# Kernel optimization log

Hardware: AMD Instinct MI355X
Metric: run time of the kernel (lower is better)

Reference implementation:

```python
import jax, jax.numpy as jnp
import numpy as np

D_MODEL = 2048
N_HEADS = 16
HEAD_DIM = D_MODEL // N_HEADS


def setup_inputs() -> dict:
    key = jax.random.key(0)
    k_x, k_wqkv, k_bqkv, k_wo, k_bo = jax.random.split(key, 5)
    B, T = 4, 1024
    s_in = 1.0 / np.sqrt(D_MODEL)
    return {
        "x": jax.random.normal(k_x, (B, T, D_MODEL), dtype=jnp.float32),
        "w_qkv": jax.random.uniform(k_wqkv, (D_MODEL, 3 * D_MODEL), jnp.float32, -s_in, s_in),
        "b_qkv": jax.random.uniform(k_bqkv, (3 * D_MODEL,), jnp.float32, -s_in, s_in),
        "w_out": jax.random.uniform(k_wo, (D_MODEL, D_MODEL), jnp.float32, -s_in, s_in),
        "b_out": jax.random.uniform(k_bo, (D_MODEL,), jnp.float32, -s_in, s_in),
    }


def reference(x, w_qkv, b_qkv, w_out, b_out) -> jnp.ndarray:
    B, T, C = x.shape
    qkv = x @ w_qkv + b_qkv                      # [B, T, 3C]
    q, k, v = jnp.split(qkv, 3, axis=-1)
    # [B, H, T, Dh]
    q = q.reshape(B, T, N_HEADS, HEAD_DIM).transpose(0, 2, 1, 3)
    k = k.reshape(B, T, N_HEADS, HEAD_DIM).transpose(0, 2, 1, 3)
    v = v.reshape(B, T, N_HEADS, HEAD_DIM).transpose(0, 2, 1, 3)
    scale = 1.0 / np.sqrt(HEAD_DIM).astype(np.float32)
    att = jnp.einsum("bhqd,bhkd->bhqk", q, k) * scale   # [B, H, T, T]
    causal = jnp.tril(jnp.ones((T, T), dtype=bool))
    att = jnp.where(causal, att, -jnp.inf)
    att = jax.nn.softmax(att, axis=-1)
    out = jnp.einsum("bhqk,bhkd->bhqd", att, v)          # [B, H, T, Dh]
    out = out.transpose(0, 2, 1, 3).reshape(B, T, C)
    return out @ w_out + b_out
```

## Files before the change

### kernel.cpp

```cpp
#include <hip/hip_runtime.h>
#include <hip/hip_bf16.h>
#include <math.h>

#define DM    2048
#define DQKV  6144
#define NH    16
#define DH    128
#define TT    1024
#define BB    4

typedef __bf16 bf16_t;
typedef __bf16 bf16x4 __attribute__((ext_vector_type(4)));
typedef __bf16 bf16x8 __attribute__((ext_vector_type(8)));
typedef float  f32x4  __attribute__((ext_vector_type(4)));

__device__ __forceinline__ void async16(const void* g, void* lds) {
  __builtin_amdgcn_global_load_lds(
      (const __attribute__((address_space(1))) unsigned int*)g,
      (__attribute__((address_space(3))) unsigned int*)lds, 16, 0, 0);
}

__global__ __launch_bounds__(256) void cast_kernel(const float* __restrict__ X,
                                                   bf16_t* __restrict__ Xb) {
  const size_t i = ((size_t)blockIdx.x * 256 + threadIdx.x) * 8;
  float4 a = *(const float4*)(X + i);
  float4 b = *(const float4*)(X + i + 4);
  bf16x8 o = {(bf16_t)a.x, (bf16_t)a.y, (bf16_t)a.z, (bf16_t)a.w,
              (bf16_t)b.x, (bf16_t)b.y, (bf16_t)b.z, (bf16_t)b.w};
  *(bf16x8*)(Xb + i) = o;
}

__global__ __launch_bounds__(256) void transpose_cast_kernel(
    const float* __restrict__ W, bf16_t* __restrict__ Wt, int K, int N) {
  __shared__ bf16_t tile[64][72];
  const int tid = threadIdx.x;
  const int tk = blockIdx.y * 64, tn = blockIdx.x * 64;
  {
    int r = tid >> 2, c0 = (tid & 3) * 16;
    const float* src = W + (size_t)(tk + r) * N + tn + c0;
#pragma unroll
    for (int j = 0; j < 4; ++j) {
      float4 v = *(const float4*)(src + j * 4);
      tile[r][c0 + j * 4 + 0] = (bf16_t)v.x;
      tile[r][c0 + j * 4 + 1] = (bf16_t)v.y;
      tile[r][c0 + j * 4 + 2] = (bf16_t)v.z;
      tile[r][c0 + j * 4 + 3] = (bf16_t)v.w;
    }
  }
  __syncthreads();
  {
    int n = tid >> 2, c0 = (tid & 3) * 16;
    bf16_t* dst = Wt + (size_t)(tn + n) * K + tk + c0;
#pragma unroll
    for (int j = 0; j < 4; ++j) {
      bf16x4 t = {tile[c0 + j * 4 + 0][n], tile[c0 + j * 4 + 1][n],
                  tile[c0 + j * 4 + 2][n], tile[c0 + j * 4 + 3][n]};
      *(bf16x4*)(dst + j * 4) = t;
    }
  }
}

__global__ __launch_bounds__(256) void v_transpose_kernel(
    const bf16_t* __restrict__ qkv, bf16_t* __restrict__ Vt_g) {
  __shared__ bf16_t tile[64][72];
  const int tid = threadIdx.x;
  const int dt = blockIdx.x;
  const int tt = blockIdx.y;
  const int bh = blockIdx.z;
  const int b = bh >> 4, h = bh & 15;
  {
    int r = tid >> 2, c0 = (tid & 3) * 16;
    const bf16_t* src =
        qkv + (size_t)(b * TT + tt * 64 + r) * DQKV + 2 * DM + h * DH + dt * 64 + c0;
    *(bf16x8*)&tile[r][c0]     = *(const bf16x8*)(src);
    *(bf16x8*)&tile[r][c0 + 8] = *(const bf16x8*)(src + 8);
  }
  __syncthreads();
  {
    int n = tid >> 2, c0 = (tid & 3) * 16;
    bf16_t* dst = Vt_g + (size_t)(bh * DH + dt * 64 + n) * TT + tt * 64 + c0;
#pragma unroll
    for (int j = 0; j < 4; ++j) {
      bf16x4 t = {tile[c0 + j * 4 + 0][n], tile[c0 + j * 4 + 1][n],
                  tile[c0 + j * 4 + 2][n], tile[c0 + j * 4 + 3][n]};
      *(bf16x4*)(dst + j * 4) = t;
    }
  }
}

template <bool OUT_BF16>
__global__ __launch_bounds__(256) void gemm_bt_kernel(
    const bf16_t* __restrict__ A, const bf16_t* __restrict__ Bt,
    const float* __restrict__ bias, void* __restrict__ out,
    int M, int N, int K) {
  __shared__ __align__(16) bf16_t As[128 * 64];
  __shared__ __align__(16) bf16_t Bs[128 * 64];

  const int tid  = threadIdx.x;
  const int lane = tid & 63;
  const int wave = tid >> 6;
  const int ln   = lane & 15;
  const int quad = lane >> 4;
  const int bm = blockIdx.y, bn = blockIdx.x;
  const int m0 = (wave >> 1) * 64;
  const int n0 = (wave & 1) * 64;

  const bf16_t* Abase = A + (size_t)bm * 128 * K;
  const bf16_t* Bbase = Bt + (size_t)bn * 128 * K;

  f32x4 acc[4][4] = {};

  const int kIters = K >> 6;
  for (int kt = 0; kt < kIters; ++kt) {
    __syncthreads();
#pragma unroll
    for (int j = 0; j < 4; ++j) {
      const int fb  = j * 256 + wave * 64;
      const int f   = fb + lane;
      const int row = f >> 3, c = f & 7;
      const int gc  = c ^ (row & 7);
      const size_t goff = (size_t)row * K + kt * 64 + gc * 8;
      async16(Abase + goff, (char*)As + fb * 16);
      async16(Bbase + goff, (char*)Bs + fb * 16);
    }
    __syncthreads();

#pragma unroll
    for (int ks = 0; ks < 2; ++ks) {
      bf16x8 af[4], bfr[4];
#pragma unroll
      for (int i = 0; i < 4; ++i) {
        int row = m0 + 16 * i + ln;
        int c = (ks * 4 + quad) ^ (row & 7);
        af[i] = *(const bf16x8*)((const char*)As + ((row * 8 + c) << 4));
      }
#pragma unroll
      for (int jj = 0; jj < 4; ++jj) {
        int row = n0 + 16 * jj + ln;
        int c = (ks * 4 + quad) ^ (row & 7);
        bfr[jj] = *(const bf16x8*)((const char*)Bs + ((row * 8 + c) << 4));
      }
#pragma unroll
      for (int i = 0; i < 4; ++i)
#pragma unroll
        for (int jj = 0; jj < 4; ++jj)
          acc[i][jj] = __builtin_amdgcn_mfma_f32_16x16x32_bf16(
              af[i], bfr[jj], acc[i][jj], 0, 0, 0);
    }
  }

#pragma unroll
  for (int i = 0; i < 4; ++i) {
    int rowg = bm * 128 + m0 + 16 * i + quad * 4;
#pragma unroll
    for (int j = 0; j < 4; ++j) {
      int colg = bn * 128 + n0 + 16 * j + ln;
      float bb = bias[colg];
#pragma unroll
      for (int r = 0; r < 4; ++r) {
        float val = acc[i][j][r] + bb;
        if (OUT_BF16)
          ((bf16_t*)out)[(size_t)(rowg + r) * N + colg] = (bf16_t)val;
        else
          ((float*)out)[(size_t)(rowg + r) * N + colg] = val;
      }
    }
  }
}

__global__ __launch_bounds__(256) void attn_kernel(
    const bf16_t* __restrict__ qkv, const bf16_t* __restrict__ Vt_g,
    bf16_t* __restrict__ attout) {
  const int bx = blockIdx.x;
  const int p  = bx & 7;
  const int h  = (bx >> 3) & 15;
  const int b  = bx >> 7;
  const int bh = b * NH + h;
  const int tid  = threadIdx.x;
  const int lane = tid & 63;
  const int wave = tid >> 6;
  const int ln   = lane & 15;
  const int quad = lane >> 4;

  __shared__ __align__(16) bf16_t Ks[2][64 * 128];
  __shared__ __align__(16) bf16_t Vs[2][128 * 64];
  __shared__ __align__(16) bf16_t Ps[4 * 16 * 64];

  const float scale = 0.08838834764831845f;

  auto prefetch = [&](int c, int bufi) {
    const int kc = c * 64;
#pragma unroll
    for (int j = 0; j < 4; ++j) {
      const int fb = j * 256 + wave * 64;
      const int l  = fb + lane;
      {
        const int row = l >> 4, cc = l & 15;
        const int gc  = cc ^ (row & 7);
        const bf16_t* g =
            qkv + (size_t)(b * TT + kc + row) * DQKV + DM + h * DH + gc * 8;
        async16(g, (char*)Ks[bufi] + fb * 16);
      }
      {
        const int d = l >> 3, cc = l & 7;
        const int gc = cc ^ (d & 7);
        const bf16_t* g = Vt_g + (size_t)(bh * DH + d) * TT + kc + gc * 8;
        async16(g, (char*)Vs[bufi] + fb * 16);
      }
    }
  };

  int buf = 0;
  prefetch(0, 0);

  for (int half = 0; half < 2; ++half) {
    const int qt = half ? (15 - p) : p;
    const int q0 = qt * 64 + wave * 16;

    bf16x8 aq[4];
    {
      const bf16_t* qrow = qkv + (size_t)(b * TT + q0 + ln) * DQKV + h * DH;
#pragma unroll
      for (int kt = 0; kt < 4; ++kt)
        aq[kt] = *(const bf16x8*)(qrow + kt * 32 + quad * 8);
    }

    f32x4 o[8] = {};
    float mrow[4], lrow[4];
#pragma unroll
    for (int r = 0; r < 4; ++r) { mrow[r] = -1e30f; lrow[r] = 0.f; }

    for (int c = 0; c <= qt; ++c) {
      const int kc = c * 64;
      __syncthreads();

      if (c < qt)                prefetch(c + 1, buf ^ 1);
      else if (half == 0)        prefetch(0,     buf ^ 1);

      const bf16_t* KsB = Ks[buf];
      const bf16_t* VsB = Vs[buf];

      f32x4 sacc[4];
#pragma unroll
      for (int jt = 0; jt < 4; ++jt) {
        sacc[jt] = (f32x4){0.f, 0.f, 0.f, 0.f};
#pragma unroll
        for (int kt = 0; kt < 4; ++kt) {
          const int row = jt * 16 + ln;
          const int sc  = (kt * 4 + quad) ^ (row & 7);
          bf16x8 bk = *(const bf16x8*)((const char*)KsB + row * 256 + sc * 16);
          sacc[jt] = __builtin_amdgcn_mfma_f32_16x16x32_bf16(aq[kt], bk,
                                                             sacc[jt], 0, 0, 0);
        }
      }

      float s[4][4], mc[4];
#pragma unroll
      for (int r = 0; r < 4; ++r) mc[r] = -1e30f;
      const bool diag = (c == qt);
#pragma unroll
      for (int jt = 0; jt < 4; ++jt) {
        int colg = kc + jt * 16 + ln;
#pragma unroll
        for (int r = 0; r < 4; ++r) {
          float sv = sacc[jt][r] * scale;
          if (diag) {
            int rowg = q0 + quad * 4 + r;
            sv = (colg <= rowg) ? sv : -1e30f;
          }
          s[jt][r] = sv;
          mc[r] = fmaxf(mc[r], sv);
        }
      }
#pragma unroll
      for (int off = 1; off < 16; off <<= 1)
#pragma unroll
        for (int r = 0; r < 4; ++r)
          mc[r] = fmaxf(mc[r], __shfl_xor(mc[r], off, 64));

      float alpha[4];
#pragma unroll
      for (int r = 0; r < 4; ++r) {
        float mnew = fmaxf(mrow[r], mc[r]);
        alpha[r] = __expf(mrow[r] - mnew);
        mrow[r] = mnew;
      }

      float rs[4] = {0.f, 0.f, 0.f, 0.f};
#pragma unroll
      for (int jt = 0; jt < 4; ++jt)
#pragma unroll
        for (int r = 0; r < 4; ++r) {
          float pv = __expf(s[jt][r] - mrow[r]);
          rs[r] += pv;
          const int row = quad * 4 + r;
          const int col = jt * 16 + ln;
          const int sc  = (col >> 3) ^ (row & 7);
          Ps[wave * 1024 + row * 64 + sc * 8 + (col & 7)] = (bf16_t)pv;
        }
#pragma unroll
      for (int off = 1; off < 16; off <<= 1)
#pragma unroll
        for (int r = 0; r < 4; ++r) rs[r] += __shfl_xor(rs[r], off, 64);
#pragma unroll
      for (int r = 0; r < 4; ++r) lrow[r] = lrow[r] * alpha[r] + rs[r];

#pragma unroll
      for (int nt = 0; nt < 8; ++nt)
#pragma unroll
        for (int r = 0; r < 4; ++r) o[nt][r] *= alpha[r];

#pragma unroll
      for (int ks = 0; ks < 2; ++ks) {
        const int psc = (ks * 4 + quad) ^ (ln & 7);
        bf16x8 ap =
            *(const bf16x8*)((const char*)Ps + wave * 2048 + ln * 128 + psc * 16);
#pragma unroll
        for (int nt = 0; nt < 8; ++nt) {
          const int row = nt * 16 + ln;
          const int sc  = (ks * 4 + quad) ^ (row & 7);
          bf16x8 bv = *(const bf16x8*)((const char*)VsB + row * 128 + sc * 16);
          o[nt] = __builtin_amdgcn_mfma_f32_16x16x32_bf16(ap, bv, o[nt], 0, 0, 0);
        }
      }
      buf ^= 1;
    }

#pragma unroll
    for (int r = 0; r < 4; ++r) {
      float inv = 1.0f / lrow[r];
      int t = q0 + quad * 4 + r;
      bf16_t* orow = attout + (size_t)(b * TT + t) * DM + h * DH;
#pragma unroll
      for (int nt = 0; nt < 8; ++nt)
        orow[nt * 16 + ln] = (bf16_t)(o[nt][r] * inv);
    }
  }
}

extern "C" void kernel_launch(void* const* d_in, const int* in_sizes, int n_in,
                              void* d_out, int out_size, void* d_ws,
                              size_t ws_size, hipStream_t stream) {
  const float* x     = (const float*)d_in[0];
  const float* w_qkv = (const float*)d_in[1];
  const float* b_qkv = (const float*)d_in[2];
  const float* w_out = (const float*)d_in[3];
  const float* b_out = (const float*)d_in[4];
  float* out = (float*)d_out;

  char* ws = (char*)d_ws;
  bf16_t* qkv    = (bf16_t*)(ws);
  bf16_t* wqkv_t = (bf16_t*)(ws + 50331648);
  bf16_t* Vt_g   = wqkv_t;
  bf16_t* wout_t = (bf16_t*)(ws + 75497472);
  bf16_t* xb     = (bf16_t*)(ws + 83886080);
  bf16_t* attout = xb;

  dim3 blk(256);
  cast_kernel<<<dim3(4096), blk, 0, stream>>>(x, xb);
  transpose_cast_kernel<<<dim3(96, 32), blk, 0, stream>>>(w_qkv, wqkv_t, 2048, 6144);
  transpose_cast_kernel<<<dim3(32, 32), blk, 0, stream>>>(w_out, wout_t, 2048, 2048);
  gemm_bt_kernel<true>
      <<<dim3(48, 32), blk, 0, stream>>>(xb, wqkv_t, b_qkv, qkv, 4096, 6144, 2048);
  v_transpose_kernel<<<dim3(2, 16, 64), blk, 0, stream>>>(qkv, Vt_g);
  attn_kernel<<<dim3(512), blk, 0, stream>>>(qkv, Vt_g, attout);
  gemm_bt_kernel<false>
      <<<dim3(16, 32), blk, 0, stream>>>(attout, wout_t, b_out, out, 4096, 2048, 2048);
}
```

Baseline: 369.3 us.

## Process both paired query tiles together to share K/V tile loads

The attention kernel previously walked the two causal-paired query tiles (p and 15-p) one after the other, reloading K/V chunks for each. It now runs a single loop over the longer tile's key chunks and computes both tiles from each shared K/V chunk, skipping the short tile once it passes its diagonal. This roughly halves K/V LDS traffic and the number of barriers, and adds launch_bounds(256,2). The cost is doubled accumulator and register state, which may raise VGPR pressure or cause spills.

```diff
diff --git a/kernel.cpp b/kernel.cpp
--- a/kernel.cpp
+++ b/kernel.cpp
@@ -168,7 +168,7 @@
   }
 }
 
-__global__ __launch_bounds__(256) void attn_kernel(
+__global__ __launch_bounds__(256, 2) void attn_kernel(
     const bf16_t* __restrict__ qkv, const bf16_t* __restrict__ Vt_g,
     bf16_t* __restrict__ attout) {
   const int bx = blockIdx.x;
@@ -184,9 +184,12 @@
 
   __shared__ __align__(16) bf16_t Ks[2][64 * 128];
   __shared__ __align__(16) bf16_t Vs[2][128 * 64];
-  __shared__ __align__(16) bf16_t Ps[4 * 16 * 64];
+  __shared__ __align__(16) bf16_t Ps[2][4 * 16 * 64];
 
   const float scale = 0.08838834764831845f;
+  const int qt0 = p, qt1 = 15 - p;
+  const int q0a = qt0 * 64 + wave * 16;
+  const int q1a = qt1 * 64 + wave * 16;
 
   auto prefetch = [&](int c, int bufi) {
     const int kc = c * 64;
@@ -210,130 +213,186 @@
     }
   };
 
+  bf16x8 aq0[4], aq1[4];
+  {
+    const bf16_t* q0r = qkv + (size_t)(b * TT + q0a + ln) * DQKV + h * DH;
+    const bf16_t* q1r = qkv + (size_t)(b * TT + q1a + ln) * DQKV + h * DH;
+#pragma unroll
+    for (int kt = 0; kt < 4; ++kt) {
+      aq0[kt] = *(const bf16x8*)(q0r + kt * 32 + quad * 8);
+      aq1[kt] = *(const bf16x8*)(q1r + kt * 32 + quad * 8);
+    }
+  }
+
+  f32x4 o0[8] = {}, o1[8] = {};
+  float m0_[4], l0_[4], m1_[4], l1_[4];
+#pragma unroll
+  for (int r = 0; r < 4; ++r) {
+    m0_[r] = -1e30f; l0_[r] = 0.f;
+    m1_[r] = -1e30f; l1_[r] = 0.f;
+  }
+
   int buf = 0;
   prefetch(0, 0);
 
-  for (int half = 0; half < 2; ++half) {
-    const int qt = half ? (15 - p) : p;
-    const int q0 = qt * 64 + wave * 16;
-
-    bf16x8 aq[4];
-    {
-      const bf16_t* qrow = qkv + (size_t)(b * TT + q0 + ln) * DQKV + h * DH;
-#pragma unroll
-      for (int kt = 0; kt < 4; ++kt)
-        aq[kt] = *(const bf16x8*)(qrow + kt * 32 + quad * 8);
-    }
-
-    f32x4 o[8] = {};
-    float mrow[4], lrow[4];
-#pragma unroll
-    for (int r = 0; r < 4; ++r) { mrow[r] = -1e30f; lrow[r] = 0.f; }
-
-    for (int c = 0; c <= qt; ++c) {
-      const int kc = c * 64;
-      __syncthreads();
-
-      if (c < qt)                prefetch(c + 1, buf ^ 1);
-      else if (half == 0)        prefetch(0,     buf ^ 1);
-
-      const bf16_t* KsB = Ks[buf];
-      const bf16_t* VsB = Vs[buf];
-
-      f32x4 sacc[4];
-#pragma unroll
-      for (int jt = 0; jt < 4; ++jt) {
-        sacc[jt] = (f32x4){0.f, 0.f, 0.f, 0.f};
-#pragma unroll
-        for (int kt = 0; kt < 4; ++kt) {
-          const int row = jt * 16 + ln;
-          const int sc  = (kt * 4 + quad) ^ (row & 7);
-          bf16x8 bk = *(const bf16x8*)((const char*)KsB + row * 256 + sc * 16);
-          sacc[jt] = __builtin_amdgcn_mfma_f32_16x16x32_bf16(aq[kt], bk,
-                                                             sacc[jt], 0, 0, 0);
-        }
-      }
-
-      float s[4][4], mc[4];
-#pragma unroll
-      for (int r = 0; r < 4; ++r) mc[r] = -1e30f;
-      const bool diag = (c == qt);
+  const int nC = qt1 + 1;
+  for (int c = 0; c < nC; ++c) {
+    const int kc = c * 64;
+    __syncthreads();
+    if (c + 1 < nC) prefetch(c + 1, buf ^ 1);
+
+    const bf16_t* KsB = Ks[buf];
+    const bf16_t* VsB = Vs[buf];
+    const bool t0 = (c <= qt0);
+
+    f32x4 sa0[4], sa1[4];
+#pragma unroll
+    for (int jt = 0; jt < 4; ++jt) {
+      sa0[jt] = (f32x4){0.f, 0.f, 0.f, 0.f};
+      sa1[jt] = (f32x4){0.f, 0.f, 0.f, 0.f};
+#pragma unroll
+      for (int kt = 0; kt < 4; ++kt) {
+        const int row = jt * 16 + ln;
+        const int sc  = (kt * 4 + quad) ^ (row & 7);
+        bf16x8 bk = *(const bf16x8*)((const char*)KsB + row * 256 + sc * 16);
+        sa1[jt] = __builtin_amdgcn_mfma_f32_16x16x32_bf16(aq1[kt], bk, sa1[jt], 0, 0, 0);
+        if (t0)
+          sa0[jt] = __builtin_amdgcn_mfma_f32_16x16x32_bf16(aq0[kt], bk, sa0[jt], 0, 0, 0);
+      }
+    }
+
+    float s1[4][4], mc1[4];
+#pragma unroll
+    for (int r = 0; r < 4; ++r) mc1[r] = -1e30f;
+    const bool diag1 = (c == qt1);
+#pragma unroll
+    for (int jt = 0; jt < 4; ++jt) {
+      int colg = kc + jt * 16 + ln;
+#pragma unroll
+      for (int r = 0; r < 4; ++r) {
+        float sv = sa1[jt][r] * scale;
+        if (diag1) sv = (colg <= q1a + quad * 4 + r) ? sv : -1e30f;
+        s1[jt][r] = sv;
+        mc1[r] = fmaxf(mc1[r], sv);
+      }
+    }
+    float s0[4][4], mc0[4];
+    if (t0) {
+#pragma unroll
+      for (int r = 0; r < 4; ++r) mc0[r] = -1e30f;
+      const bool diag0 = (c == qt0);
 #pragma unroll
       for (int jt = 0; jt < 4; ++jt) {
         int colg = kc + jt * 16 + ln;
 #pragma unroll
         for (int r = 0; r < 4; ++r) {
-          float sv = sacc[jt][r] * scale;
-          if (diag) {
-            int rowg = q0 + quad * 4 + r;
-            sv = (colg <= rowg) ? sv : -1e30f;
-          }
-          s[jt][r] = sv;
-          mc[r] = fmaxf(mc[r], sv);
+          float sv = sa0[jt][r] * scale;
+          if (diag0) sv = (colg <= q0a + quad * 4 + r) ? sv : -1e30f;
+          s0[jt][r] = sv;
+          mc0[r] = fmaxf(mc0[r], sv);
         }
       }
-#pragma unroll
-      for (int off = 1; off < 16; off <<= 1)
-#pragma unroll
-        for (int r = 0; r < 4; ++r)
-          mc[r] = fmaxf(mc[r], __shfl_xor(mc[r], off, 64));
-
-      float alpha[4];
-#pragma unroll
-      for (int r = 0; r < 4; ++r) {
-        float mnew = fmaxf(mrow[r], mc[r]);
-        alpha[r] = __expf(mrow[r] - mnew);
-        mrow[r] = mnew;
-      }
-
-      float rs[4] = {0.f, 0.f, 0.f, 0.f};
-#pragma unroll
-      for (int jt = 0; jt < 4; ++jt)
-#pragma unroll
-        for (int r = 0; r < 4; ++r) {
-          float pv = __expf(s[jt][r] - mrow[r]);
-          rs[r] += pv;
-          const int row = quad * 4 + r;
-          const int col = jt * 16 + ln;
-          const int sc  = (col >> 3) ^ (row & 7);
-          Ps[wave * 1024 + row * 64 + sc * 8 + (col & 7)] = (bf16_t)pv;
+    }
+#pragma unroll
+    for (int off = 1; off < 16; off <<= 1) {
+#pragma unroll
+      for (int r = 0; r < 4; ++r) {
+        mc1[r] = fmaxf(mc1[r], __shfl_xor(mc1[r], off, 64));
+        if (t0) mc0[r] = fmaxf(mc0[r], __shfl_xor(mc0[r], off, 64));
+      }
+    }
+
+    float a1[4], a0[4];
+#pragma unroll
+    for (int r = 0; r < 4; ++r) {
+      float mn = fmaxf(m1_[r], mc1[r]);
+      a1[r] = __expf(m1_[r] - mn);
+      m1_[r] = mn;
+    }
+    if (t0) {
+#pragma unroll
+      for (int r = 0; r < 4; ++r) {
+        float mn = fmaxf(m0_[r], mc0[r]);
+        a0[r] = __expf(m0_[r] - mn);
+        m0_[r] = mn;
+      }
+    }
+
+    float rs1[4] = {0.f, 0.f, 0.f, 0.f}, rs0[4] = {0.f, 0.f, 0.f, 0.f};
+#pragma unroll
+    for (int jt = 0; jt < 4; ++jt) {
+#pragma unroll
+      for (int r = 0; r < 4; ++r) {
+        const int row = quad * 4 + r;
+        const int col = jt * 16 + ln;
+        const int sc  = (col >> 3) ^ (row & 7);
+        float pv = __expf(s1[jt][r] - m1_[r]);
+        rs1[r] += pv;
+        Ps[1][wave * 1024 + row * 64 + sc * 8 + (col & 7)] = (bf16_t)pv;
+        if (t0) {
+          float pw = __expf(s0[jt][r] - m0_[r]);
+          rs0[r] += pw;
+          Ps[0][wave * 1024 + row * 64 + sc * 8 + (col & 7)] = (bf16_t)pw;
         }
-#pragma unroll
-      for (int off = 1; off < 16; off <<= 1)
-#pragma unroll
-        for (int r = 0; r < 4; ++r) rs[r] += __shfl_xor(rs[r], off, 64);
-#pragma unroll
-      for (int r = 0; r < 4; ++r) lrow[r] = lrow[r] * alpha[r] + rs[r];
-
+      }
+    }
+#pragma unroll
+    for (int off = 1; off < 16; off <<= 1) {
+#pragma unroll
+      for (int r = 0; r < 4; ++r) {
+        rs1[r] += __shfl_xor(rs1[r], off, 64);
+        if (t0) rs0[r] += __shfl_xor(rs0[r], off, 64);
+      }
+    }
+#pragma unroll
+    for (int r = 0; r < 4; ++r) l1_[r] = l1_[r] * a1[r] + rs1[r];
+    if (t0) {
+#pragma unroll
+      for (int r = 0; r < 4; ++r) l0_[r] = l0_[r] * a0[r] + rs0[r];
+    }
+
+#pragma unroll
+    for (int nt = 0; nt < 8; ++nt)
+#pragma unroll
+      for (int r = 0; r < 4; ++r) o1[nt][r] *= a1[r];
+    if (t0) {
 #pragma unroll
       for (int nt = 0; nt < 8; ++nt)
 #pragma unroll
-        for (int r = 0; r < 4; ++r) o[nt][r] *= alpha[r];
-
-#pragma unroll
-      for (int ks = 0; ks < 2; ++ks) {
-        const int psc = (ks * 4 + quad) ^ (ln & 7);
-        bf16x8 ap =
-            *(const bf16x8*)((const char*)Ps + wave * 2048 + ln * 128 + psc * 16);
-#pragma unroll
-        for (int nt = 0; nt < 8; ++nt) {
-          const int row = nt * 16 + ln;
-          const int sc  = (ks * 4 + quad) ^ (row & 7);
-          bf16x8 bv = *(const bf16x8*)((const char*)VsB + row * 128 + sc * 16);
-          o[nt] = __builtin_amdgcn_mfma_f32_16x16x32_bf16(ap, bv, o[nt], 0, 0, 0);
-        }
-      }
-      buf ^= 1;
-    }
-
-#pragma unroll
-    for (int r = 0; r < 4; ++r) {
-      float inv = 1.0f / lrow[r];
-      int t = q0 + quad * 4 + r;
-      bf16_t* orow = attout + (size_t)(b * TT + t) * DM + h * DH;
-#pragma unroll
-      for (int nt = 0; nt < 8; ++nt)
-        orow[nt * 16 + ln] = (bf16_t)(o[nt][r] * inv);
+        for (int r = 0; r < 4; ++r) o0[nt][r] *= a0[r];
+    }
+
+#pragma unroll
+    for (int ks = 0; ks < 2; ++ks) {
+      const int psc = (ks * 4 + quad) ^ (ln & 7);
+      bf16x8 ap1 =
+          *(const bf16x8*)((const char*)&Ps[1][0] + wave * 2048 + ln * 128 + psc * 16);
+      bf16x8 ap0;
+      if (t0)
+        ap0 = *(const bf16x8*)((const char*)&Ps[0][0] + wave * 2048 + ln * 128 + psc * 16);
+#pragma unroll
+      for (int nt = 0; nt < 8; ++nt) {
+        const int row = nt * 16 + ln;
+        const int sc  = (ks * 4 + quad) ^ (row & 7);
+        bf16x8 bv = *(const bf16x8*)((const char*)VsB + row * 128 + sc * 16);
+        o1[nt] = __builtin_amdgcn_mfma_f32_16x16x32_bf16(ap1, bv, o1[nt], 0, 0, 0);
+        if (t0)
+          o0[nt] = __builtin_amdgcn_mfma_f32_16x16x32_bf16(ap0, bv, o0[nt], 0, 0, 0);
+      }
+    }
+    buf ^= 1;
+  }
+
+#pragma unroll
+  for (int r = 0; r < 4; ++r) {
+    float inv1 = 1.0f / l1_[r];
+    float inv0 = 1.0f / l0_[r];
+    bf16_t* or1 = attout + (size_t)(b * TT + q1a + quad * 4 + r) * DM + h * DH;
+    bf16_t* or0 = attout + (size_t)(b * TT + q0a + quad * 4 + r) * DM + h * DH;
+#pragma unroll
+    for (int nt = 0; nt < 8; ++nt) {
+      or1[nt * 16 + ln] = (bf16_t)(o1[nt][r] * inv1);
+      or0[nt * 16 + ln] = (bf16_t)(o0[nt][r] * inv0);
     }
   }
 }
```

After: 725.8 us. +96.5%, slower.

## Split attention into one block per query tile, single-buffered LDS, higher occupancy

Applied to the files above, without the earlier changes.

The attention kernel now launches one block per (batch-head, query tile) instead of pairing two complementary query tiles per block, which doubles the grid to 1024 blocks. Heavy tiles are ordered first to help load balance. The K/V double buffer becomes a single buffer, roughly halving LDS per block, and launch_bounds requests 4 blocks per CU so more waves can be resident. The trade-off is losing the explicit prefetch overlap: each step now loads K/V and waits at a barrier before computing, so latency hiding relies on occupancy across blocks.

```diff
diff --git a/kernel.cpp b/kernel.cpp
--- a/kernel.cpp
+++ b/kernel.cpp
@@ -168,28 +168,44 @@
   }
 }
 
-__global__ __launch_bounds__(256) void attn_kernel(
+__global__ __launch_bounds__(256, 4) void attn_kernel(
     const bf16_t* __restrict__ qkv, const bf16_t* __restrict__ Vt_g,
     bf16_t* __restrict__ attout) {
   const int bx = blockIdx.x;
-  const int p  = bx & 7;
-  const int h  = (bx >> 3) & 15;
-  const int b  = bx >> 7;
-  const int bh = b * NH + h;
+  const int bh = bx & 63;
+  const int qt = 15 - (bx >> 6);
+  const int b  = bh >> 4;
+  const int h  = bh & 15;
   const int tid  = threadIdx.x;
   const int lane = tid & 63;
   const int wave = tid >> 6;
   const int ln   = lane & 15;
   const int quad = lane >> 4;
 
-  __shared__ __align__(16) bf16_t Ks[2][64 * 128];
-  __shared__ __align__(16) bf16_t Vs[2][128 * 64];
+  __shared__ __align__(16) bf16_t Ks[64 * 128];
+  __shared__ __align__(16) bf16_t Vs[128 * 64];
   __shared__ __align__(16) bf16_t Ps[4 * 16 * 64];
 
   const float scale = 0.08838834764831845f;
-
-  auto prefetch = [&](int c, int bufi) {
+  const int q0 = qt * 64 + wave * 16;
+
+  bf16x8 aq[4];
+  {
+    const bf16_t* qrow = qkv + (size_t)(b * TT + q0 + ln) * DQKV + h * DH;
+#pragma unroll
+    for (int kt = 0; kt < 4; ++kt)
+      aq[kt] = *(const bf16x8*)(qrow + kt * 32 + quad * 8);
+  }
+
+  f32x4 o[8] = {};
+  float mrow[4], lrow[4];
+#pragma unroll
+  for (int r = 0; r < 4; ++r) { mrow[r] = -1e30f; lrow[r] = 0.f; }
+
+  for (int c = 0; c <= qt; ++c) {
     const int kc = c * 64;
+    __syncthreads();
+
 #pragma unroll
     for (int j = 0; j < 4; ++j) {
       const int fb = j * 256 + wave * 64;
@@ -199,142 +215,107 @@
         const int gc  = cc ^ (row & 7);
         const bf16_t* g =
             qkv + (size_t)(b * TT + kc + row) * DQKV + DM + h * DH + gc * 8;
-        async16(g, (char*)Ks[bufi] + fb * 16);
+        async16(g, (char*)Ks + fb * 16);
       }
       {
         const int d = l >> 3, cc = l & 7;
         const int gc = cc ^ (d & 7);
         const bf16_t* g = Vt_g + (size_t)(bh * DH + d) * TT + kc + gc * 8;
-        async16(g, (char*)Vs[bufi] + fb * 16);
-      }
-    }
-  };
-
-  int buf = 0;
-  prefetch(0, 0);
-
-  for (int half = 0; half < 2; ++half) {
-    const int qt = half ? (15 - p) : p;
-    const int q0 = qt * 64 + wave * 16;
-
-    bf16x8 aq[4];
-    {
-      const bf16_t* qrow = qkv + (size_t)(b * TT + q0 + ln) * DQKV + h * DH;
-#pragma unroll
-      for (int kt = 0; kt < 4; ++kt)
-        aq[kt] = *(const bf16x8*)(qrow + kt * 32 + quad * 8);
-    }
-
-    f32x4 o[8] = {};
-    float mrow[4], lrow[4];
-#pragma unroll
-    for (int r = 0; r < 4; ++r) { mrow[r] = -1e30f; lrow[r] = 0.f; }
-
-    for (int c = 0; c <= qt; ++c) {
-      const int kc = c * 64;
-      __syncthreads();
-
-      if (c < qt)                prefetch(c + 1, buf ^ 1);
-      else if (half == 0)        prefetch(0,     buf ^ 1);
-
-      const bf16_t* KsB = Ks[buf];
-      const bf16_t* VsB = Vs[buf];
-
-      f32x4 sacc[4];
-#pragma unroll
-      for (int jt = 0; jt < 4; ++jt) {
-        sacc[jt] = (f32x4){0.f, 0.f, 0.f, 0.f};
-#pragma unroll
-        for (int kt = 0; kt < 4; ++kt) {
-          const int row = jt * 16 + ln;
-          const int sc  = (kt * 4 + quad) ^ (row & 7);
-          bf16x8 bk = *(const bf16x8*)((const char*)KsB + row * 256 + sc * 16);
-          sacc[jt] = __builtin_amdgcn_mfma_f32_16x16x32_bf16(aq[kt], bk,
-                                                             sacc[jt], 0, 0, 0);
-        }
-      }
-
-      float s[4][4], mc[4];
-#pragma unroll
-      for (int r = 0; r < 4; ++r) mc[r] = -1e30f;
-      const bool diag = (c == qt);
-#pragma unroll
-      for (int jt = 0; jt < 4; ++jt) {
-        int colg = kc + jt * 16 + ln;
-#pragma unroll
-        for (int r = 0; r < 4; ++r) {
-          float sv = sacc[jt][r] * scale;
-          if (diag) {
-            int rowg = q0 + quad * 4 + r;
-            sv = (colg <= rowg) ? sv : -1e30f;
-          }
-          s[jt][r] = sv;
-          mc[r] = fmaxf(mc[r], sv);
-        }
-      }
-#pragma unroll
-      for (int off = 1; off < 16; off <<= 1)
-#pragma unroll
-        for (int r = 0; r < 4; ++r)
-          mc[r] = fmaxf(mc[r], __shfl_xor(mc[r], off, 64));
-
-      float alpha[4];
+        async16(g, (char*)Vs + fb * 16);
+      }
+    }
+    __syncthreads();
+
+    f32x4 sacc[4];
+#pragma unroll
+    for (int jt = 0; jt < 4; ++jt) {
+      sacc[jt] = (f32x4){0.f, 0.f, 0.f, 0.f};
+#pragma unroll
+      for (int kt = 0; kt < 4; ++kt) {
+        const int row = jt * 16 + ln;
+        const int sc  = (kt * 4 + quad) ^ (row & 7);
+        bf16x8 bk = *(const bf16x8*)((const char*)Ks + row * 256 + sc * 16);
+        sacc[jt] = __builtin_amdgcn_mfma_f32_16x16x32_bf16(aq[kt], bk,
+                                                           sacc[jt], 0, 0, 0);
+      }
+    }
+
+    float s[4][4], mc[4];
+#pragma unroll
+    for (int r = 0; r < 4; ++r) mc[r] = -1e30f;
+    const bool diag = (c == qt);
+#pragma unroll
+    for (int jt = 0; jt < 4; ++jt) {
+      int colg = kc + jt * 16 + ln;
 #pragma unroll
       for (int r = 0; r < 4; ++r) {
-        float mnew = fmaxf(mrow[r], mc[r]);
-        alpha[r] = __expf(mrow[r] - mnew);
-        mrow[r] = mnew;
-      }
-
-      float rs[4] = {0.f, 0.f, 0.f, 0.f};
-#pragma unroll
-      for (int jt = 0; jt < 4; ++jt)
-#pragma unroll
-        for (int r = 0; r < 4; ++r) {
-          float pv = __expf(s[jt][r] - mrow[r]);
-          rs[r] += pv;
-          const int row = quad * 4 + r;
-          const int col = jt * 16 + ln;
-          const int sc  = (col >> 3) ^ (row & 7);
-          Ps[wave * 1024 + row * 64 + sc * 8 + (col & 7)] = (bf16_t)pv;
-        }
-#pragma unroll
-      for (int off = 1; off < 16; off <<= 1)
-#pragma unroll
-        for (int r = 0; r < 4; ++r) rs[r] += __shfl_xor(rs[r], off, 64);
-#pragma unroll
-      for (int r = 0; r < 4; ++r) lrow[r] = lrow[r] * alpha[r] + rs[r];
-
-#pragma unroll
-      for (int nt = 0; nt < 8; ++nt)
-#pragma unroll
-        for (int r = 0; r < 4; ++r) o[nt][r] *= alpha[r];
-
-#pragma unroll
-      for (int ks = 0; ks < 2; ++ks) {
-        const int psc = (ks * 4 + quad) ^ (ln & 7);
-        bf16x8 ap =
-            *(const bf16x8*)((const char*)Ps + wave * 2048 + ln * 128 + psc * 16);
-#pragma unroll
-        for (int nt = 0; nt < 8; ++nt) {
-          const int row = nt * 16 + ln;
-          const int sc  = (ks * 4 + quad) ^ (row & 7);
-          bf16x8 bv = *(const bf16x8*)((const char*)VsB + row * 128 + sc * 16);
-          o[nt] = __builtin_amdgcn_mfma_f32_16x16x32_bf16(ap, bv, o[nt], 0, 0, 0);
-        }
-      }
-      buf ^= 1;
-    }
-
+        float sv = sacc[jt][r] * scale;
+        if (diag) sv = (colg <= q0 + quad * 4 + r) ? sv : -1e30f;
+        s[jt][r] = sv;
+        mc[r] = fmaxf(mc[r], sv);
+      }
+    }
+#pragma unroll
+    for (int off = 1; off < 16; off <<= 1)
+#pragma unroll
+      for (int r = 0; r < 4; ++r)
+        mc[r] = fmaxf(mc[r], __shfl_xor(mc[r], off, 64));
+
+    float alpha[4];
 #pragma unroll
     for (int r = 0; r < 4; ++r) {
-      float inv = 1.0f / lrow[r];
-      int t = q0 + quad * 4 + r;
-      bf16_t* orow = attout + (size_t)(b * TT + t) * DM + h * DH;
-#pragma unroll
-      for (int nt = 0; nt < 8; ++nt)
-        orow[nt * 16 + ln] = (bf16_t)(o[nt][r] * inv);
-    }
+      float mn = fmaxf(mrow[r], mc[r]);
+      alpha[r] = __expf(mrow[r] - mn);
+      mrow[r] = mn;
+    }
+
+    float rs[4] = {0.f, 0.f, 0.f, 0.f};
+#pragma unroll
+    for (int jt = 0; jt < 4; ++jt)
+#pragma unroll
+      for (int r = 0; r < 4; ++r) {
+        float pv = __expf(s[jt][r] - mrow[r]);
+        rs[r] += pv;
+        const int row = quad * 4 + r;
+        const int col = jt * 16 + ln;
+        const int sc  = (col >> 3) ^ (row & 7);
+        Ps[wave * 1024 + row * 64 + sc * 8 + (col & 7)] = (bf16_t)pv;
+      }
+#pragma unroll
+    for (int off = 1; off < 16; off <<= 1)
+#pragma unroll
+      for (int r = 0; r < 4; ++r) rs[r] += __shfl_xor(rs[r], off, 64);
+#pragma unroll
+    for (int r = 0; r < 4; ++r) lrow[r] = lrow[r] * alpha[r] + rs[r];
+
+#pragma unroll
+    for (int nt = 0; nt < 8; ++nt)
+#pragma unroll
+      for (int r = 0; r < 4; ++r) o[nt][r] *= alpha[r];
+
+#pragma unroll
+    for (int ks = 0; ks < 2; ++ks) {
+      const int psc = (ks * 4 + quad) ^ (ln & 7);
+      bf16x8 ap =
+          *(const bf16x8*)((const char*)Ps + wave * 2048 + ln * 128 + psc * 16);
+#pragma unroll
+      for (int nt = 0; nt < 8; ++nt) {
+        const int row = nt * 16 + ln;
+        const int sc  = (ks * 4 + quad) ^ (row & 7);
+        bf16x8 bv = *(const bf16x8*)((const char*)Vs + row * 128 + sc * 16);
+        o[nt] = __builtin_amdgcn_mfma_f32_16x16x32_bf16(ap, bv, o[nt], 0, 0, 0);
+      }
+    }
+  }
+
+#pragma unroll
+  for (int r = 0; r < 4; ++r) {
+    float inv = 1.0f / lrow[r];
+    int t = q0 + quad * 4 + r;
+    bf16_t* orow = attout + (size_t)(b * TT + t) * DM + h * DH;
+#pragma unroll
+    for (int nt = 0; nt < 8; ++nt)
+      orow[nt * 16 + ln] = (bf16_t)(o[nt][r] * inv);
   }
 }
 
@@ -363,7 +344,7 @@
   gemm_bt_kernel<true>
       <<<dim3(48, 32), blk, 0, stream>>>(xb, wqkv_t, b_qkv, qkv, 4096, 6144, 2048);
   v_transpose_kernel<<<dim3(2, 16, 64), blk, 0, stream>>>(qkv, Vt_g);
-  attn_kernel<<<dim3(512), blk, 0, stream>>>(qkv, Vt_g, attout);
+  attn_kernel<<<dim3(1024), blk, 0, stream>>>(qkv, Vt_g, attout);
   gemm_bt_kernel<false>
       <<<dim3(16, 32), blk, 0, stream>>>(attout, wout_t, b_out, out, 4096, 2048, 2048);
 }
```

After: 375.5 us. No clear change (+1.7%).
